# Kernel tuning notes

Hardware: AMD Instinct MI355X
Metric: run time of the kernel (lower is better)

Reference implementation:

```python
import jax, jax.numpy as jnp
import numpy as np

V, H, S, B, T = 32000, 1024, 512, 16, 128
SOS = 1  # config['special_tokens']['SOS'] assumed = 1


def setup_inputs() -> dict:
    key = jax.random.key(0)
    ks = jax.random.split(key, 16)
    s = 0.02
    return {
        "encoder_outputs": jax.random.normal(ks[0], (B, S, H), jnp.float32),
        "encoder_h": jax.random.normal(ks[1], (1, B, H), jnp.float32),
        "encoder_c": jax.random.normal(ks[2], (1, B, H), jnp.float32),
        "embedding": jax.random.normal(ks[3], (V, H), jnp.float32) * s,
        "Wq": jax.random.normal(ks[4], (H, H), jnp.float32) * s,
        "bq": jnp.zeros((H,), jnp.float32),
        "Wk": jax.random.normal(ks[5], (H, H), jnp.float32) * s,
        "bk": jnp.zeros((H,), jnp.float32),
        "Wv": jax.random.normal(ks[6], (H, H), jnp.float32) * s,
        "bv": jnp.zeros((H,), jnp.float32),
        "W_ih": jax.random.normal(ks[7], (4 * H, 2 * H), jnp.float32) * s,
        "b_ih": jnp.zeros((4 * H,), jnp.float32),
        "W_hh": jax.random.normal(ks[8], (4 * H, H), jnp.float32) * s,
        "b_hh": jnp.zeros((4 * H,), jnp.float32),
        "W_out": jax.random.normal(ks[9], (V, H), jnp.float32) * s,
        "b_out": jnp.zeros((V,), jnp.float32),
    }


def reference(encoder_outputs, encoder_h, encoder_c, embedding,
              Wq, bq, Wk, bk, Wv, bv,
              W_ih, b_ih, W_hh, b_hh, W_out, b_out):
    h0 = encoder_h[0]  # [B,H]
    c0 = encoder_c[0]
    # key/value projections of encoder outputs are constant across steps
    K = jnp.einsum('bsh,dh->bsd', encoder_outputs, Wk) + bk   # [B,S,H]
    Vl = jnp.einsum('bsh,dh->bsd', encoder_outputs, Wv) + bv  # [B,S,H]
    # decoder input is always SOS (source never updates it when target_tensor is None)
    emb = jnp.broadcast_to(embedding[SOS], (h0.shape[0], H))  # [B,H]
    scale = 1.0 / jnp.sqrt(jnp.float32(H))
    # 1x1 look-ahead mask (query seq_len == 1) is a no-op -> omitted

    def step(carry, _):
        h, c = carry
        q = h @ Wq.T + bq                                 # [B,H]
        scores = jnp.einsum('bh,bsh->bs', q, K) * scale   # [B,S]
        w = jax.nn.softmax(scores, axis=-1)
        ctx = jnp.einsum('bs,bsh->bh', w, Vl)             # [B,H]
        x = jnp.concatenate([emb, ctx], axis=-1)          # [B,2H] (embedded, attn)
        gates = x @ W_ih.T + b_ih + h @ W_hh.T + b_hh     # [B,4H]
        i, f, g, o = jnp.split(gates, 4, axis=-1)         # torch LSTM gate order i,f,g,o
        c2 = jax.nn.sigmoid(f) * c + jax.nn.sigmoid(i) * jnp.tanh(g)
        h2 = jax.nn.sigmoid(o) * jnp.tanh(c2)
        logits = h2 @ W_out.T + b_out                     # [B,V]
        return (h2, c2), logits

    (hT, cT), outs = jax.lax.scan(step, (h0, c0), None, length=T)  # outs [T,B,V]
    outs = jnp.transpose(outs, (1, 0, 2))                          # [B,T,V]
    log_probs = jax.nn.log_softmax(outs, axis=-1)
    return log_probs, (hT[None], cT[None])
```

## Files before the change

kernel.cpp:

```cpp
#include <hip/hip_runtime.h>
#include <hip/hip_bf16.h>
#include <math.h>

typedef short short8 __attribute__((ext_vector_type(8)));
typedef short short4v __attribute__((ext_vector_type(4)));
typedef float f32x4 __attribute__((ext_vector_type(4)));
typedef unsigned long long u64;

#define DEVI __device__ __forceinline__

DEVI float bf2f(short s){ union{unsigned u; float f;} x; x.u = ((unsigned)(unsigned short)s) << 16; return x.f; }

DEVI void st_u32v(unsigned* p, unsigned v){ __hip_atomic_store(p, v, __ATOMIC_RELAXED, __HIP_MEMORY_SCOPE_SYSTEM); }
DEVI u64  ld_u64v(const u64* p){ return __hip_atomic_load(p, __ATOMIC_RELAXED, __HIP_MEMORY_SCOPE_SYSTEM); }
DEVI unsigned bfbits(float f){ __hip_bfloat16 h = __float2bfloat16(f); unsigned short b; __builtin_memcpy(&b,&h,2); return (unsigned)b; }

constexpr size_t o_wout   = 0;
constexpr size_t o_encbf  = 0;
constexpr size_t o_kbf    = 16777216;
constexpr size_t o_wkbf   = 33554432;
constexpr size_t o_wvbf   = 35651584;
constexpr size_t o_wqtbf  = 37748736;
constexpr size_t o_vt     = 41943040;
constexpr size_t o_kq     = 65536000;
constexpr size_t o_vbf    = o_kq    + 16777216;
constexpr size_t o_wih2   = o_vbf   + 16777216;
constexpr size_t o_whh    = o_wih2  + 8388608;
constexpr size_t o_hall   = o_whh   + 8388608;
constexpr size_t o_gconst = o_hall  + 4194304;
constexpr size_t o_sb     = o_gconst+ 16384;
constexpr size_t o_hg     = o_sb    + 32768;
constexpr size_t o_ctxn   = o_hg    + 65536;
constexpr size_t o_eg     = o_ctxn  + 65536;

__global__ void k_convert(const float* __restrict__ src, __hip_bfloat16* __restrict__ dst, int n){
  int i = (blockIdx.x*blockDim.x + threadIdx.x)*4;
  int stride = gridDim.x*blockDim.x*4;
  for (; i < n; i += stride){
    float4 v = *(const float4*)(src+i);
    __hip_bfloat16 o[4] = {__float2bfloat16(v.x),__float2bfloat16(v.y),__float2bfloat16(v.z),__float2bfloat16(v.w)};
    *(short4v*)(dst+i) = *(const short4v*)o;
  }
}

__global__ void k_tcvt(const float* __restrict__ src, __hip_bfloat16* __restrict__ dst){
  __shared__ float tile[64][65];
  int i0 = blockIdx.y*64, j0 = blockIdx.x*64;
  int tr = threadIdx.x >> 6, tc = threadIdx.x & 63;
  for (int p=0;p<16;p++){ int r = p*4 + tr; tile[r][tc] = src[(size_t)(i0+r)*1024 + j0+tc]; }
  __syncthreads();
  for (int p=0;p<16;p++){ int r = p*4 + tr; dst[(size_t)(j0+r)*1024 + i0+tc] = __float2bfloat16(tile[tc][r]); }
}

__global__ void k_extract(const float* __restrict__ src, __hip_bfloat16* __restrict__ dst){
  int i = blockIdx.x*blockDim.x + threadIdx.x;
  int stride = gridDim.x*blockDim.x;
  for (; i < 4096*1024; i += stride){
    int r = i >> 10, c = i & 1023;
    dst[i] = __float2bfloat16(src[((size_t)r << 11) + 1024 + c]);
  }
}

__global__ void k_init(const float* __restrict__ eh, unsigned* __restrict__ h2,
                       unsigned* __restrict__ zbase){
  int i = blockIdx.x*blockDim.x + threadIdx.x;
  if (i < 16384) h2[i] = bfbits(eh[i]);
  if (i < 24576) zbase[i] = 0u;
}

__global__ void k_gconst(const float* __restrict__ emb, const float* __restrict__ Wih,
                         const float* __restrict__ bih, const float* __restrict__ bhh,
                         float* __restrict__ gc){
  int w = threadIdx.x >> 6, lane = threadIdx.x & 63;
  int n = blockIdx.x*4 + w;
  const float* er = emb + 1024;
  const float* wr = Wih + (size_t)n*2048;
  float acc = 0.f;
  for (int q=0;q<16;q++){ int k = lane*16+q; acc += er[k]*wr[k]; }
  for (int off=32; off; off>>=1) acc += __shfl_xor(acc, off);
  if (lane==0) gc[n] = acc + bih[n] + bhh[n];
}

__global__ void k_sb(const __hip_bfloat16* __restrict__ Kb, const float* __restrict__ bq,
                     float* __restrict__ sb){
  int w = threadIdx.x >> 6, lane = threadIdx.x & 63;
  int r = blockIdx.x*4 + w;
  const __hip_bfloat16* kr = Kb + (size_t)r*1024;
  float acc = 0.f;
  for (int q=0;q<16;q++){ int k = lane*16+q; acc += __bfloat162float(kr[k])*bq[k]; }
  for (int off=32; off; off>>=1) acc += __shfl_xor(acc, off);
  if (lane==0) sb[r] = acc * 0.03125f;
}

__global__ void k_vtrans(const __hip_bfloat16* __restrict__ V, __hip_bfloat16* __restrict__ VT){
  __shared__ short t[64][65];
  int b = blockIdx.z, s0 = blockIdx.y*64, h0 = blockIdx.x*64;
  int r = threadIdx.x >> 6, c = threadIdx.x & 63;
  const short* vp = (const short*)V + ((size_t)(b*512 + s0))*1024 + h0;
  #pragma unroll
  for (int p=0;p<16;p++) t[p*4+r][c] = vp[(size_t)(p*4+r)*1024 + c];
  __syncthreads();
  short* op = (short*)VT + ((size_t)(b*1024 + h0))*512 + s0;
  #pragma unroll
  for (int p=0;p<16;p++) op[(size_t)(p*4+r)*512 + c] = t[c][p*4+r];
}

template<int EPI>
__global__ __launch_bounds__(256) void k_gemm(const __hip_bfloat16* __restrict__ A,
    const __hip_bfloat16* __restrict__ Bm, const float* __restrict__ bias,
    void* __restrict__ Cp, int M, int N, int K, float scale){
  __shared__ __hip_bfloat16 sA[128*40];
  __shared__ __hip_bfloat16 sB[128*40];
  int tid = threadIdx.x;
  int lane = tid & 63, w = tid >> 6;
  int wr = w >> 1, wc = w & 1;
  int m0 = blockIdx.y*128, n0 = blockIdx.x*128;
  int lrow = lane & 15, lk = lane >> 4;
  f32x4 acc[4][4] = {};
  for (int k0 = 0; k0 < K; k0 += 32){
    __syncthreads();
    #pragma unroll
    for (int l0 = 0; l0 < 1024; l0 += 256){
      int l = l0 + tid;
      int half = l >> 9;
      int ch = l & 511;
      int row = ch >> 2, seg = ch & 3;
      const __hip_bfloat16* src = half ? (Bm + (size_t)(n0+row)*K + k0 + seg*8)
                                       : (A  + (size_t)(m0+row)*K + k0 + seg*8);
      __hip_bfloat16* dst = (half ? sB : sA) + row*40 + seg*8;
      *(short8*)dst = *(const short8*)src;
    }
    __syncthreads();
    short8 af[4], bfq[4];
    #pragma unroll
    for (int mi=0;mi<4;mi++) af[mi]  = *(short8*)(sA + (wr*64+mi*16+lrow)*40 + lk*8);
    #pragma unroll
    for (int ni=0;ni<4;ni++) bfq[ni] = *(short8*)(sB + (wc*64+ni*16+lrow)*40 + lk*8);
    #pragma unroll
    for (int mi=0;mi<4;mi++)
      #pragma unroll
      for (int ni=0;ni<4;ni++)
        acc[mi][ni] = __builtin_amdgcn_mfma_f32_16x16x32_bf16(af[mi], bfq[ni], acc[mi][ni], 0,0,0);
  }
  int crow0 = (lane>>4)*4;
  int ccol = lane & 15;
  #pragma unroll
  for (int mi=0;mi<4;mi++)
    #pragma unroll
    for (int ni=0;ni<4;ni++){
      int gn = n0 + wc*64 + ni*16 + ccol;
      float bv = bias ? bias[gn] : 0.0f;
      #pragma unroll
      for (int j=0;j<4;j++){
        int gm = m0 + wr*64 + mi*16 + crow0 + j;
        float v = acc[mi][ni][j]*scale + bv;
        if (EPI==0){
          ((__hip_bfloat16*)Cp)[(size_t)gm*N + gn] = __float2bfloat16(v);
        } else {
          int tt = gm >> 4, bb = gm & 15;
          ((float*)Cp)[(size_t)(bb*128+tt)*N + gn] = v;
        }
      }
    }
}

__global__ __launch_bounds__(256, 1) void k_decode(
    const __hip_bfloat16* __restrict__ KQ, const __hip_bfloat16* __restrict__ VT,
    const float* __restrict__ sb, const __hip_bfloat16* __restrict__ Whh,
    const __hip_bfloat16* __restrict__ Wih2, const float* __restrict__ gconst,
    const float* __restrict__ ec,
    unsigned* __restrict__ h2v, unsigned* __restrict__ egv,
    unsigned* __restrict__ ctx2v, __hip_bfloat16* __restrict__ hall,
    float* __restrict__ outH, float* __restrict__ outC)
{
  __shared__ __attribute__((aligned(16))) __hip_bfloat16 h4L[4][1032];
  __shared__ __attribute__((aligned(16))) float eL[528];
  __shared__ __attribute__((aligned(16))) float sPf[1024];
  __shared__ __attribute__((aligned(16))) __hip_bfloat16 sCtx[64];
  __shared__ float sSb[32];
  __shared__ float sGc[64];
  __shared__ float sRed[4];

  const int tid = threadIdx.x;
  const int lane = tid & 63, wv = tid >> 6;
  const int l16 = lane & 15, lhi = lane >> 4;
  const int blk = blockIdx.x;
  const int xcd = blk & 7, slot = blk >> 3;
  const int grp = xcd >> 1, half = xcd & 1;
  const int bloc = half*2 + (slot >> 4);
  const int chunk = slot & 15;
  const int g4 = grp*4;
  const int b = g4 + bloc;
  const int j0 = (half*32 + slot) * 16;

  short8 wfrag[64];
  {
    const __hip_bfloat16* wsrc = (wv < 2) ? Whh : Wih2;
    const int koff = (wv & 1) * 512;
    #pragma unroll
    for (int tt = 0; tt < 4; tt++)
      #pragma unroll
      for (int kt = 0; kt < 16; kt++)
        wfrag[tt*16+kt] = *(const short8*)(wsrc + (size_t)(tt*1024 + j0 + l16)*1024 + koff + kt*32 + lhi*8);
  }
  if (tid < 32) sSb[tid] = sb[b*512 + chunk*32 + tid];
  if (tid < 64) sGc[(tid>>4)*16 + (tid&15)] = gconst[(tid>>4)*1024 + j0 + (tid&15)];
  float creg = 0.f;
  if (tid < 64) creg = ec[(size_t)(g4 + (tid>>4))*1024 + j0 + (tid&15)];

  const __hip_bfloat16* kqBlk = KQ + ((size_t)(b*512 + chunk*32))*1024;
  const int ar = (l16 < 4) ? l16 : 3;
  const short8 zfrag = {};
  f32x4 gacc[4] = {};

  for (int st = 0; st < 128; ++st){
    const unsigned wantH = (unsigned)st;
    const unsigned wantE = (unsigned)(st+1);
    const unsigned wantC = (unsigned)(st+1);

    {
      const u64* s0 = (const u64*)(h2v + (size_t)b*1024) + tid*2;
      u64 a0, a1; bool ok;
      do {
        a0 = ld_u64v(s0); a1 = ld_u64v(s0+1);
        ok = (((unsigned)a0>>16)==wantH) && ((unsigned)(a0>>48)==wantH)
          && (((unsigned)a1>>16)==wantH) && ((unsigned)(a1>>48)==wantH);
      } while(!ok);
      short4v o = { (short)(unsigned)a0, (short)(a0>>32), (short)(unsigned)a1, (short)(a1>>32) };
      *(short4v*)&h4L[bloc][tid*4] = o;
    }
    __syncthreads();
    {
      int row = tid >> 3, kx = tid & 7;
      const __hip_bfloat16* kp = kqBlk + (size_t)row*1024 + kx*8;
      float acc = 0.f;
      #pragma unroll
      for (int q = 0; q < 16; q++){
        short8 kv = *(const short8*)(kp + q*64);
        short8 hv = *(const short8*)&h4L[bloc][kx*8 + q*64];
        #pragma unroll
        for (int e2 = 0; e2 < 8; e2++) acc += bf2f(hv[e2]) * bf2f(kv[e2]);
      }
      acc += __shfl_xor(acc, 1); acc += __shfl_xor(acc, 2); acc += __shfl_xor(acc, 4);
      if (kx == 0)
        st_u32v(&egv[b*512 + chunk*32 + row], bfbits(expf(acc + sSb[row])) | (wantE<<16));
    }
    {
      const u64* sp0 = (const u64*)(h2v + (size_t)(g4 + ((bloc+1)&3))*1024) + tid*2;
      const u64* sp1 = (const u64*)(h2v + (size_t)(g4 + ((bloc+2)&3))*1024) + tid*2;
      const u64* sp2 = (const u64*)(h2v + (size_t)(g4 + ((bloc+3)&3))*1024) + tid*2;
      u64 v[6]; bool ok;
      do {
        v[0]=ld_u64v(sp0); v[1]=ld_u64v(sp0+1);
        v[2]=ld_u64v(sp1); v[3]=ld_u64v(sp1+1);
        v[4]=ld_u64v(sp2); v[5]=ld_u64v(sp2+1);
        ok = true;
        #pragma unroll
        for (int i=0;i<6;i++) ok &= (((unsigned)v[i]>>16)==wantH) && ((unsigned)(v[i]>>48)==wantH);
      } while(!ok);
      #pragma unroll
      for (int rr=0;rr<3;rr++){
        int rl = (bloc+rr+1)&3;
        short4v o = { (short)(unsigned)v[rr*2], (short)(v[rr*2]>>32),
                      (short)(unsigned)v[rr*2+1], (short)(v[rr*2+1]>>32) };
        *(short4v*)&h4L[rl][tid*4] = o;
      }
    }
    __syncthreads();
    if (wv < 2){
      const int ko = (wv & 1) * 512;
      #pragma unroll
      for (int kt = 0; kt < 16; kt++){
        short8 a = *(const short8*)&h4L[ar][ko + kt*32 + lhi*8];
        a = (l16 < 4) ? a : zfrag;
        #pragma unroll
        for (int tt = 0; tt < 4; tt++)
          gacc[tt] = __builtin_amdgcn_mfma_f32_16x16x32_bf16(a, wfrag[tt*16+kt], gacc[tt], 0,0,0);
      }
    }

    {
      const u64* s = (const u64*)(egv + b*512) + tid;
      u64 v;
      do { v = ld_u64v(s); }
      while(!((((unsigned)v>>16)==wantE) && ((unsigned)(v>>48)==wantE)));
      float e0 = bf2f((short)(unsigned)v), e1 = bf2f((short)(v>>32));
      int i0 = tid*2;
      int pad = (i0>>7)<<2;
      eL[i0 + pad] = e0; eL[i0+1 + pad] = e1;
      float lp = e0 + e1;
      for (int off=32; off; off>>=1) lp += __shfl_xor(lp, off);
      if (lane == 0) sRed[wv] = lp;
    }
    __syncthreads();
    {
      float Linv = 1.0f/(sRed[0]+sRed[1]+sRed[2]+sRed[3]);
      int hloc = tid >> 2, sc = (tid & 3)*128;
      const __hip_bfloat16* vp = VT + ((size_t)(b*1024 + chunk*64 + hloc))*512 + sc;
      const float* ep = eL + sc + ((sc>>7)<<2);
      float a = 0.f;
      #pragma unroll
      for (int q = 0; q < 16; q++){
        short8 vv = *(const short8*)(vp + q*8);
        float4 e0 = *(const float4*)(ep + q*8);
        float4 e1 = *(const float4*)(ep + q*8 + 4);
        a += e0.x*bf2f(vv[0]) + e0.y*bf2f(vv[1]) + e0.z*bf2f(vv[2]) + e0.w*bf2f(vv[3]);
        a += e1.x*bf2f(vv[4]) + e1.y*bf2f(vv[5]) + e1.z*bf2f(vv[6]) + e1.w*bf2f(vv[7]);
      }
      a += __shfl_xor(a, 1); a += __shfl_xor(a, 2);
      if ((tid & 3) == 0) sCtx[hloc] = __float2bfloat16(a * Linv);
    }
    __syncthreads();
    if (tid < 64){
      unsigned short cbts; __builtin_memcpy(&cbts, &sCtx[tid], 2);
      st_u32v(&ctx2v[(size_t)b*1024 + chunk*64 + tid], (unsigned)cbts | (wantC<<16));
    }

    {
      int r = tid >> 6, c0 = (tid & 63)*16;
      const u64* s = (const u64*)(ctx2v + (size_t)(g4 + r)*1024 + c0);
      u64 v[8]; bool ok;
      do {
        ok = true;
        #pragma unroll
        for (int i=0;i<8;i++) v[i] = ld_u64v(s+i);
        #pragma unroll
        for (int i=0;i<8;i++) ok &= (((unsigned)v[i]>>16)==wantC) && ((unsigned)(v[i]>>48)==wantC);
      } while(!ok);
      short8 o0, o1;
      #pragma unroll
      for (int i=0;i<4;i++){ o0[2*i] = (short)(unsigned)v[i]; o0[2*i+1] = (short)(v[i]>>32); }
      #pragma unroll
      for (int i=0;i<4;i++){ o1[2*i] = (short)(unsigned)v[4+i]; o1[2*i+1] = (short)(v[4+i]>>32); }
      *(short8*)&h4L[r][c0] = o0;
      *(short8*)&h4L[r][c0+8] = o1;
    }
    __syncthreads();
    if (wv >= 2){
      const int ko = (wv & 1) * 512;
      #pragma unroll
      for (int kt = 0; kt < 16; kt++){
        short8 a = *(const short8*)&h4L[ar][ko + kt*32 + lhi*8];
        a = (l16 < 4) ? a : zfrag;
        #pragma unroll
        for (int tt = 0; tt < 4; tt++)
          gacc[tt] = __builtin_amdgcn_mfma_f32_16x16x32_bf16(a, wfrag[tt*16+kt], gacc[tt], 0,0,0);
      }
    }
    if (lhi == 0){
      #pragma unroll
      for (int tt = 0; tt < 4; tt++)
        *(f32x4*)&sPf[(wv*64 + tt*16 + l16)*4] = gacc[tt];
    }
    #pragma unroll
    for (int tt = 0; tt < 4; tt++) gacc[tt] = (f32x4){0.f,0.f,0.f,0.f};
    __syncthreads();
    if (tid < 64){
      int bb = tid >> 4, jj = tid & 15;
      float gv[4];
      #pragma unroll
      for (int tt = 0; tt < 4; tt++){
        float s = sGc[tt*16 + jj];
        #pragma unroll
        for (int w2 = 0; w2 < 4; w2++) s += sPf[(w2*64 + tt*16 + jj)*4 + bb];
        gv[tt] = s;
      }
      float si = 1.f/(1.f+expf(-gv[0]));
      float sf = 1.f/(1.f+expf(-gv[1]));
      float so = 1.f/(1.f+expf(-gv[3]));
      float c2 = sf*creg + si*tanhf(gv[2]);
      float h2 = so*tanhf(c2);
      creg = c2;
      int gb = g4 + bb;
      __hip_bfloat16 hbv = __float2bfloat16(h2);
      unsigned short hbits; __builtin_memcpy(&hbits, &hbv, 2);
      st_u32v(&h2v[(size_t)gb*1024 + j0 + jj], (unsigned)hbits | ((unsigned)(st+1)<<16));
      hall[((size_t)(st*16 + gb))*1024 + j0 + jj] = hbv;
      if (st == 127){ outH[gb*1024 + j0 + jj] = h2; outC[gb*1024 + j0 + jj] = c2; }
    }
  }
}

__global__ __launch_bounds__(256) void k_logsm(float* __restrict__ out){
  int row = blockIdx.x;
  float* p = out + (size_t)row*32000;
  int tid = threadIdx.x;
  __shared__ float red[4];
  float s = 0.f;
  for (int i = tid*4; i < 32000; i += 1024){
    float4 v = *(float4*)(p+i);
    s += __expf(v.x)+__expf(v.y)+__expf(v.z)+__expf(v.w);
  }
  for (int off=32; off; off>>=1) s += __shfl_xor(s, off);
  if ((tid&63)==0) red[tid>>6] = s;
  __syncthreads();
  float L = logf(red[0]+red[1]+red[2]+red[3]);
  for (int i = tid*4; i < 32000; i += 1024){
    float4 v = *(float4*)(p+i);
    v.x-=L; v.y-=L; v.z-=L; v.w-=L;
    *(float4*)(p+i) = v;
  }
}

extern "C" void kernel_launch(void* const* d_in, const int* in_sizes, int n_in,
                              void* d_out, int out_size, void* d_ws, size_t ws_size,
                              hipStream_t stream){
  const float* enc = (const float*)d_in[0];
  const float* eh  = (const float*)d_in[1];
  const float* ec  = (const float*)d_in[2];
  const float* emb = (const float*)d_in[3];
  const float* Wq  = (const float*)d_in[4];
  const float* bq  = (const float*)d_in[5];
  const float* Wk  = (const float*)d_in[6];
  const float* bk  = (const float*)d_in[7];
  const float* Wv  = (const float*)d_in[8];
  const float* bv  = (const float*)d_in[9];
  const float* Wih = (const float*)d_in[10];
  const float* bih = (const float*)d_in[11];
  const float* Whh = (const float*)d_in[12];
  const float* bhh = (const float*)d_in[13];
  const float* Wo  = (const float*)d_in[14];
  const float* bo  = (const float*)d_in[15];

  char* ws = (char*)d_ws;
  __hip_bfloat16* encbf = (__hip_bfloat16*)(ws + o_encbf);
  __hip_bfloat16* kbf   = (__hip_bfloat16*)(ws + o_kbf);
  __hip_bfloat16* wkbf  = (__hip_bfloat16*)(ws + o_wkbf);
  __hip_bfloat16* wvbf  = (__hip_bfloat16*)(ws + o_wvbf);
  __hip_bfloat16* wqtbf = (__hip_bfloat16*)(ws + o_wqtbf);
  __hip_bfloat16* vt    = (__hip_bfloat16*)(ws + o_vt);
  __hip_bfloat16* woutbf= (__hip_bfloat16*)(ws + o_wout);
  __hip_bfloat16* kq    = (__hip_bfloat16*)(ws + o_kq);
  __hip_bfloat16* vbf   = (__hip_bfloat16*)(ws + o_vbf);
  __hip_bfloat16* wih2  = (__hip_bfloat16*)(ws + o_wih2);
  __hip_bfloat16* whhbf = (__hip_bfloat16*)(ws + o_whh);
  __hip_bfloat16* hall  = (__hip_bfloat16*)(ws + o_hall);
  float* gconst = (float*)(ws + o_gconst);
  float* sbp    = (float*)(ws + o_sb);
  unsigned* h2v   = (unsigned*)(ws + o_hg);
  unsigned* ctx2v = (unsigned*)(ws + o_ctxn);
  unsigned* egv   = (unsigned*)(ws + o_eg);
  float* outP   = (float*)d_out;
  float* outH   = outP + 65536000;
  float* outC   = outH + 16384;

  k_convert<<<1024,256,0,stream>>>(enc, encbf, 8388608);
  k_convert<<<256,256,0,stream>>>(Wk, wkbf, 1048576);
  k_convert<<<256,256,0,stream>>>(Wv, wvbf, 1048576);
  k_tcvt<<<dim3(16,16),256,0,stream>>>(Wq, wqtbf);
  k_gemm<0><<<dim3(8,64),256,0,stream>>>(encbf, wkbf, bk, kbf, 8192,1024,1024, 1.f);
  k_gemm<0><<<dim3(8,64),256,0,stream>>>(encbf, wvbf, bv, vbf, 8192,1024,1024, 1.f);
  k_gemm<0><<<dim3(8,64),256,0,stream>>>(kbf, wqtbf, (const float*)nullptr, kq, 8192,1024,1024, 0.03125f);
  k_vtrans<<<dim3(16,8,16),256,0,stream>>>(vbf, vt);
  k_sb<<<2048,256,0,stream>>>(kbf, bq, sbp);
  k_extract<<<1024,256,0,stream>>>(Wih, wih2);
  k_convert<<<1024,256,0,stream>>>(Whh, whhbf, 4194304);
  k_gconst<<<1024,256,0,stream>>>(emb, Wih, bih, bhh, gconst);
  k_init<<<96,256,0,stream>>>(eh, h2v, ctx2v);

  {
    const __hip_bfloat16* a_kq = kq; const __hip_bfloat16* a_vt = vt;
    const float* a_sb = sbp; const __hip_bfloat16* a_whh = whhbf;
    const __hip_bfloat16* a_wih = wih2; const float* a_gc = gconst;
    const float* a_ec = ec;
    unsigned* a_h = h2v; unsigned* a_e = egv; unsigned* a_c = ctx2v;
    __hip_bfloat16* a_ha = hall;
    float* a_oh = outH; float* a_oc = outC;
    void* args[] = { &a_kq, &a_vt, &a_sb, &a_whh, &a_wih, &a_gc, &a_ec,
                     &a_h, &a_e, &a_c, &a_ha, &a_oh, &a_oc };
    hipError_t err = hipLaunchCooperativeKernel((void*)k_decode, dim3(256), dim3(256),
                                                args, 0u, stream);
    if (err != hipSuccess){
      k_decode<<<256,256,0,stream>>>(kq, vt, sbp, whhbf, wih2, gconst, ec,
                                     h2v, egv, ctx2v, hall, outH, outC);
    }
  }

  k_convert<<<2048,256,0,stream>>>(Wo, woutbf, 32768000);
  k_gemm<1><<<dim3(250,16),256,0,stream>>>(hall, woutbf, bo, d_out, 2048,32000,1024, 1.f);
  k_logsm<<<2048,256,0,stream>>>(outP);
}
```

Before: 2.733 ms.

## Decouple attention batch ownership from gate group and overlap W_hh gates with next step

Each block now runs attention for its own batch row (bown) but computes LSTM gates for a different group of four rows (gg = ga+2). This lets the recurrent W_hh·h contribution for the next step be computed right after h is published, instead of waiting on the critical path next to the context. The h/e/ctx exchange buffers are double-buffered by step parity, and the W_hh vs W_ih wave roles are swapped. It adds an extra grid-wide h wait and synchronisation per step, plus more flag traffic across XCDs.

```diff
diff --git a/kernel.cpp b/kernel.cpp
--- a/kernel.cpp
+++ b/kernel.cpp
@@ -29,9 +29,9 @@
 constexpr size_t o_hall   = o_whh   + 8388608;
 constexpr size_t o_gconst = o_hall  + 4194304;
 constexpr size_t o_sb     = o_gconst+ 16384;
-constexpr size_t o_hg     = o_sb    + 32768;
-constexpr size_t o_ctxn   = o_hg    + 65536;
-constexpr size_t o_eg     = o_ctxn  + 65536;
+constexpr size_t o_hv     = o_sb    + 32768;
+constexpr size_t o_ev     = o_hv    + 131072;
+constexpr size_t o_cv     = o_ev    + 65536;
 
 __global__ void k_convert(const float* __restrict__ src, __hip_bfloat16* __restrict__ dst, int n){
   int i = (blockIdx.x*blockDim.x + threadIdx.x)*4;
@@ -61,11 +61,10 @@
   }
 }
 
-__global__ void k_init(const float* __restrict__ eh, unsigned* __restrict__ h2,
-                       unsigned* __restrict__ zbase){
+__global__ void k_init(const float* __restrict__ eh, unsigned* __restrict__ base){
   int i = blockIdx.x*blockDim.x + threadIdx.x;
-  if (i < 16384) h2[i] = bfbits(eh[i]);
-  if (i < 24576) zbase[i] = 0u;
+  if (i < 16384) base[i] = bfbits(eh[i]);
+  else if (i < 81920) base[i] = 0u;
 }
 
 __global__ void k_gconst(const float* __restrict__ emb, const float* __restrict__ Wih,
@@ -169,8 +168,8 @@
     const float* __restrict__ sb, const __hip_bfloat16* __restrict__ Whh,
     const __hip_bfloat16* __restrict__ Wih2, const float* __restrict__ gconst,
     const float* __restrict__ ec,
-    unsigned* __restrict__ h2v, unsigned* __restrict__ egv,
-    unsigned* __restrict__ ctx2v, __hip_bfloat16* __restrict__ hall,
+    unsigned* __restrict__ hv, unsigned* __restrict__ ev,
+    unsigned* __restrict__ cv, __hip_bfloat16* __restrict__ hall,
     float* __restrict__ outH, float* __restrict__ outC)
 {
   __shared__ __attribute__((aligned(16))) __hip_bfloat16 h4L[4][1032];
@@ -186,16 +185,16 @@
   const int l16 = lane & 15, lhi = lane >> 4;
   const int blk = blockIdx.x;
   const int xcd = blk & 7, slot = blk >> 3;
-  const int grp = xcd >> 1, half = xcd & 1;
-  const int bloc = half*2 + (slot >> 4);
+  const int ga = xcd >> 1, half = xcd & 1;
+  const int bown = ga*4 + half*2 + (slot >> 4);
   const int chunk = slot & 15;
-  const int g4 = grp*4;
-  const int b = g4 + bloc;
+  const int gg = (ga + 2) & 3;
+  const int g4 = gg*4;
   const int j0 = (half*32 + slot) * 16;
 
   short8 wfrag[64];
   {
-    const __hip_bfloat16* wsrc = (wv < 2) ? Whh : Wih2;
+    const __hip_bfloat16* wsrc = (wv >= 2) ? Whh : Wih2;
     const int koff = (wv & 1) * 512;
     #pragma unroll
     for (int tt = 0; tt < 4; tt++)
@@ -203,23 +202,61 @@
       for (int kt = 0; kt < 16; kt++)
         wfrag[tt*16+kt] = *(const short8*)(wsrc + (size_t)(tt*1024 + j0 + l16)*1024 + koff + kt*32 + lhi*8);
   }
-  if (tid < 32) sSb[tid] = sb[b*512 + chunk*32 + tid];
+  if (tid < 32) sSb[tid] = sb[bown*512 + chunk*32 + tid];
   if (tid < 64) sGc[(tid>>4)*16 + (tid&15)] = gconst[(tid>>4)*1024 + j0 + (tid&15)];
   float creg = 0.f;
   if (tid < 64) creg = ec[(size_t)(g4 + (tid>>4))*1024 + j0 + (tid&15)];
 
-  const __hip_bfloat16* kqBlk = KQ + ((size_t)(b*512 + chunk*32))*1024;
+  const __hip_bfloat16* kqBlk = KQ + ((size_t)(bown*512 + chunk*32))*1024;
   const int ar = (l16 < 4) ? l16 : 3;
   const short8 zfrag = {};
   f32x4 gacc[4] = {};
 
+  {
+    int r = tid >> 6, c0 = (tid & 63)*16;
+    const u64* s = (const u64*)(hv + (size_t)(g4 + r)*1024 + c0);
+    u64 v[8]; bool ok;
+    do {
+      ok = true;
+      #pragma unroll
+      for (int i=0;i<8;i++) v[i] = ld_u64v(s+i);
+      #pragma unroll
+      for (int i=0;i<8;i++) ok &= (((unsigned)v[i]>>16)==0u) && ((unsigned)(v[i]>>48)==0u);
+    } while(!ok);
+    #pragma unroll
+    for (int i=0;i<8;i++){
+      short2 o = { (short)(unsigned)v[i], (short)(v[i]>>32) };
+      *(short2*)&h4L[r][c0 + 2*i] = *(short2*)&o;
+    }
+  }
+  __syncthreads();
+  if (wv >= 2){
+    const int ko = (wv & 1) * 512;
+    #pragma unroll
+    for (int kt = 0; kt < 16; kt++){
+      short8 a = *(const short8*)&h4L[ar][ko + kt*32 + lhi*8];
+      a = (l16 < 4) ? a : zfrag;
+      #pragma unroll
+      for (int tt = 0; tt < 4; tt++)
+        gacc[tt] = __builtin_amdgcn_mfma_f32_16x16x32_bf16(a, wfrag[tt*16+kt], gacc[tt], 0,0,0);
+    }
+    if (lhi == 0){
+      #pragma unroll
+      for (int tt = 0; tt < 4; tt++)
+        *(f32x4*)&sPf[(wv*64 + tt*16 + l16)*4] = gacc[tt];
+    }
+    #pragma unroll
+    for (int tt = 0; tt < 4; tt++) gacc[tt] = (f32x4){0.f,0.f,0.f,0.f};
+  }
+  __syncthreads();
+
   for (int st = 0; st < 128; ++st){
+    const int p0 = st & 1, p1 = (st+1) & 1;
     const unsigned wantH = (unsigned)st;
-    const unsigned wantE = (unsigned)(st+1);
-    const unsigned wantC = (unsigned)(st+1);
+    const unsigned wantN = (unsigned)(st+1);
 
     {
-      const u64* s0 = (const u64*)(h2v + (size_t)b*1024) + tid*2;
+      const u64* s0 = (const u64*)(hv + (size_t)p0*16384 + (size_t)bown*1024) + tid*2;
       u64 a0, a1; bool ok;
       do {
         a0 = ld_u64v(s0); a1 = ld_u64v(s0+1);
@@ -227,7 +264,7 @@
           && (((unsigned)a1>>16)==wantH) && ((unsigned)(a1>>48)==wantH);
       } while(!ok);
       short4v o = { (short)(unsigned)a0, (short)(a0>>32), (short)(unsigned)a1, (short)(a1>>32) };
-      *(short4v*)&h4L[bloc][tid*4] = o;
+      *(short4v*)&h4L[0][tid*4] = o;
     }
     __syncthreads();
     {
@@ -237,56 +274,22 @@
       #pragma unroll
       for (int q = 0; q < 16; q++){
         short8 kv = *(const short8*)(kp + q*64);
-        short8 hv = *(const short8*)&h4L[bloc][kx*8 + q*64];
-        #pragma unroll
-        for (int e2 = 0; e2 < 8; e2++) acc += bf2f(hv[e2]) * bf2f(kv[e2]);
+        short8 hv8 = *(const short8*)&h4L[0][kx*8 + q*64];
+        #pragma unroll
+        for (int e2 = 0; e2 < 8; e2++) acc += bf2f(hv8[e2]) * bf2f(kv[e2]);
       }
       acc += __shfl_xor(acc, 1); acc += __shfl_xor(acc, 2); acc += __shfl_xor(acc, 4);
       if (kx == 0)
-        st_u32v(&egv[b*512 + chunk*32 + row], bfbits(expf(acc + sSb[row])) | (wantE<<16));
-    }
+        st_u32v(&ev[(size_t)p1*8192 + bown*512 + chunk*32 + row], bfbits(expf(acc + sSb[row])) | (wantN<<16));
+    }
+
     {
-      const u64* sp0 = (const u64*)(h2v + (size_t)(g4 + ((bloc+1)&3))*1024) + tid*2;
-      const u64* sp1 = (const u64*)(h2v + (size_t)(g4 + ((bloc+2)&3))*1024) + tid*2;
-      const u64* sp2 = (const u64*)(h2v + (size_t)(g4 + ((bloc+3)&3))*1024) + tid*2;
-      u64 v[6]; bool ok;
-      do {
-        v[0]=ld_u64v(sp0); v[1]=ld_u64v(sp0+1);
-        v[2]=ld_u64v(sp1); v[3]=ld_u64v(sp1+1);
-        v[4]=ld_u64v(sp2); v[5]=ld_u64v(sp2+1);
-        ok = true;
-        #pragma unroll
-        for (int i=0;i<6;i++) ok &= (((unsigned)v[i]>>16)==wantH) && ((unsigned)(v[i]>>48)==wantH);
-      } while(!ok);
-      #pragma unroll
-      for (int rr=0;rr<3;rr++){
-        int rl = (bloc+rr+1)&3;
-        short4v o = { (short)(unsigned)v[rr*2], (short)(v[rr*2]>>32),
-                      (short)(unsigned)v[rr*2+1], (short)(v[rr*2+1]>>32) };
-        *(short4v*)&h4L[rl][tid*4] = o;
-      }
-    }
-    __syncthreads();
-    if (wv < 2){
-      const int ko = (wv & 1) * 512;
-      #pragma unroll
-      for (int kt = 0; kt < 16; kt++){
-        short8 a = *(const short8*)&h4L[ar][ko + kt*32 + lhi*8];
-        a = (l16 < 4) ? a : zfrag;
-        #pragma unroll
-        for (int tt = 0; tt < 4; tt++)
-          gacc[tt] = __builtin_amdgcn_mfma_f32_16x16x32_bf16(a, wfrag[tt*16+kt], gacc[tt], 0,0,0);
-      }
-    }
-
-    {
-      const u64* s = (const u64*)(egv + b*512) + tid;
+      const u64* s = (const u64*)(ev + (size_t)p1*8192 + bown*512) + tid;
       u64 v;
       do { v = ld_u64v(s); }
-      while(!((((unsigned)v>>16)==wantE) && ((unsigned)(v>>48)==wantE)));
+      while(!((((unsigned)v>>16)==wantN) && ((unsigned)(v>>48)==wantN)));
       float e0 = bf2f((short)(unsigned)v), e1 = bf2f((short)(v>>32));
-      int i0 = tid*2;
-      int pad = (i0>>7)<<2;
+      int i0 = tid*2, pad = (tid>>6)<<2;
       eL[i0 + pad] = e0; eL[i0+1 + pad] = e1;
       float lp = e0 + e1;
       for (int off=32; off; off>>=1) lp += __shfl_xor(lp, off);
@@ -296,14 +299,14 @@
     {
       float Linv = 1.0f/(sRed[0]+sRed[1]+sRed[2]+sRed[3]);
       int hloc = tid >> 2, sc = (tid & 3)*128;
-      const __hip_bfloat16* vp = VT + ((size_t)(b*1024 + chunk*64 + hloc))*512 + sc;
-      const float* ep = eL + sc + ((sc>>7)<<2);
+      const __hip_bfloat16* vp = VT + ((size_t)(bown*1024 + chunk*64 + hloc))*512 + sc;
+      const float* epp = eL + sc + ((sc>>7)<<2);
       float a = 0.f;
       #pragma unroll
       for (int q = 0; q < 16; q++){
         short8 vv = *(const short8*)(vp + q*8);
-        float4 e0 = *(const float4*)(ep + q*8);
-        float4 e1 = *(const float4*)(ep + q*8 + 4);
+        float4 e0 = *(const float4*)(epp + q*8);
+        float4 e1 = *(const float4*)(epp + q*8 + 4);
         a += e0.x*bf2f(vv[0]) + e0.y*bf2f(vv[1]) + e0.z*bf2f(vv[2]) + e0.w*bf2f(vv[3]);
         a += e1.x*bf2f(vv[4]) + e1.y*bf2f(vv[5]) + e1.z*bf2f(vv[6]) + e1.w*bf2f(vv[7]);
       }
@@ -313,30 +316,28 @@
     __syncthreads();
     if (tid < 64){
       unsigned short cbts; __builtin_memcpy(&cbts, &sCtx[tid], 2);
-      st_u32v(&ctx2v[(size_t)b*1024 + chunk*64 + tid], (unsigned)cbts | (wantC<<16));
+      st_u32v(&cv[(size_t)p1*16384 + (size_t)bown*1024 + chunk*64 + tid], (unsigned)cbts | (wantN<<16));
     }
 
     {
       int r = tid >> 6, c0 = (tid & 63)*16;
-      const u64* s = (const u64*)(ctx2v + (size_t)(g4 + r)*1024 + c0);
+      const u64* s = (const u64*)(cv + (size_t)p1*16384 + (size_t)(g4 + r)*1024 + c0);
       u64 v[8]; bool ok;
       do {
         ok = true;
         #pragma unroll
         for (int i=0;i<8;i++) v[i] = ld_u64v(s+i);
         #pragma unroll
-        for (int i=0;i<8;i++) ok &= (((unsigned)v[i]>>16)==wantC) && ((unsigned)(v[i]>>48)==wantC);
+        for (int i=0;i<8;i++) ok &= (((unsigned)v[i]>>16)==wantN) && ((unsigned)(v[i]>>48)==wantN);
       } while(!ok);
-      short8 o0, o1;
-      #pragma unroll
-      for (int i=0;i<4;i++){ o0[2*i] = (short)(unsigned)v[i]; o0[2*i+1] = (short)(v[i]>>32); }
-      #pragma unroll
-      for (int i=0;i<4;i++){ o1[2*i] = (short)(unsigned)v[4+i]; o1[2*i+1] = (short)(v[4+i]>>32); }
-      *(short8*)&h4L[r][c0] = o0;
-      *(short8*)&h4L[r][c0+8] = o1;
-    }
-    __syncthreads();
-    if (wv >= 2){
+      #pragma unroll
+      for (int i=0;i<8;i++){
+        short2 o = { (short)(unsigned)v[i], (short)(v[i]>>32) };
+        *(short2*)&h4L[r][c0 + 2*i] = *(short2*)&o;
+      }
+    }
+    __syncthreads();
+    if (wv < 2){
       const int ko = (wv & 1) * 512;
       #pragma unroll
       for (int kt = 0; kt < 16; kt++){
@@ -346,14 +347,14 @@
         for (int tt = 0; tt < 4; tt++)
           gacc[tt] = __builtin_amdgcn_mfma_f32_16x16x32_bf16(a, wfrag[tt*16+kt], gacc[tt], 0,0,0);
       }
-    }
-    if (lhi == 0){
-      #pragma unroll
-      for (int tt = 0; tt < 4; tt++)
-        *(f32x4*)&sPf[(wv*64 + tt*16 + l16)*4] = gacc[tt];
-    }
-    #pragma unroll
-    for (int tt = 0; tt < 4; tt++) gacc[tt] = (f32x4){0.f,0.f,0.f,0.f};
+      if (lhi == 0){
+        #pragma unroll
+        for (int tt = 0; tt < 4; tt++)
+          *(f32x4*)&sPf[(wv*64 + tt*16 + l16)*4] = gacc[tt];
+      }
+      #pragma unroll
+      for (int tt = 0; tt < 4; tt++) gacc[tt] = (f32x4){0.f,0.f,0.f,0.f};
+    }
     __syncthreads();
     if (tid < 64){
       int bb = tid >> 4, jj = tid & 15;
@@ -372,11 +373,51 @@
       float h2 = so*tanhf(c2);
       creg = c2;
       int gb = g4 + bb;
-      __hip_bfloat16 hbv = __float2bfloat16(h2);
-      unsigned short hbits; __builtin_memcpy(&hbits, &hbv, 2);
-      st_u32v(&h2v[(size_t)gb*1024 + j0 + jj], (unsigned)hbits | ((unsigned)(st+1)<<16));
+      unsigned hb = bfbits(h2);
+      st_u32v(&hv[(size_t)p1*16384 + (size_t)gb*1024 + j0 + jj], hb | (wantN<<16));
+      __hip_bfloat16 hbv; unsigned short hu = (unsigned short)hb; __builtin_memcpy(&hbv, &hu, 2);
       hall[((size_t)(st*16 + gb))*1024 + j0 + jj] = hbv;
       if (st == 127){ outH[gb*1024 + j0 + jj] = h2; outC[gb*1024 + j0 + jj] = c2; }
+    }
+
+    if (st < 127){
+      {
+        int r = tid >> 6, c0 = (tid & 63)*16;
+        const u64* s = (const u64*)(hv + (size_t)p1*16384 + (size_t)(g4 + r)*1024 + c0);
+        u64 v[8]; bool ok;
+        do {
+          ok = true;
+          #pragma unroll
+          for (int i=0;i<8;i++) v[i] = ld_u64v(s+i);
+          #pragma unroll
+          for (int i=0;i<8;i++) ok &= (((unsigned)v[i]>>16)==wantN) && ((unsigned)(v[i]>>48)==wantN);
+        } while(!ok);
+        #pragma unroll
+        for (int i=0;i<8;i++){
+          short2 o = { (short)(unsigned)v[i], (short)(v[i]>>32) };
+          *(short2*)&h4L[r][c0 + 2*i] = *(short2*)&o;
+        }
+      }
+      __syncthreads();
+      if (wv >= 2){
+        const int ko = (wv & 1) * 512;
+        #pragma unroll
+        for (int kt = 0; kt < 16; kt++){
+          short8 a = *(const short8*)&h4L[ar][ko + kt*32 + lhi*8];
+          a = (l16 < 4) ? a : zfrag;
+          #pragma unroll
+          for (int tt = 0; tt < 4; tt++)
+            gacc[tt] = __builtin_amdgcn_mfma_f32_16x16x32_bf16(a, wfrag[tt*16+kt], gacc[tt], 0,0,0);
+        }
+        if (lhi == 0){
+          #pragma unroll
+          for (int tt = 0; tt < 4; tt++)
+            *(f32x4*)&sPf[(wv*64 + tt*16 + l16)*4] = gacc[tt];
+        }
+        #pragma unroll
+        for (int tt = 0; tt < 4; tt++) gacc[tt] = (f32x4){0.f,0.f,0.f,0.f};
+      }
+      __syncthreads();
     }
   }
 }
@@ -437,9 +478,9 @@
   __hip_bfloat16* hall  = (__hip_bfloat16*)(ws + o_hall);
   float* gconst = (float*)(ws + o_gconst);
   float* sbp    = (float*)(ws + o_sb);
-  unsigned* h2v   = (unsigned*)(ws + o_hg);
-  unsigned* ctx2v = (unsigned*)(ws + o_ctxn);
-  unsigned* egv   = (unsigned*)(ws + o_eg);
+  unsigned* hvp = (unsigned*)(ws + o_hv);
+  unsigned* evp = (unsigned*)(ws + o_ev);
+  unsigned* cvp = (unsigned*)(ws + o_cv);
   float* outP   = (float*)d_out;
   float* outH   = outP + 65536000;
   float* outC   = outH + 16384;
@@ -456,14 +497,14 @@
   k_extract<<<1024,256,0,stream>>>(Wih, wih2);
   k_convert<<<1024,256,0,stream>>>(Whh, whhbf, 4194304);
   k_gconst<<<1024,256,0,stream>>>(emb, Wih, bih, bhh, gconst);
-  k_init<<<96,256,0,stream>>>(eh, h2v, ctx2v);
+  k_init<<<320,256,0,stream>>>(eh, hvp);
 
   {
     const __hip_bfloat16* a_kq = kq; const __hip_bfloat16* a_vt = vt;
     const float* a_sb = sbp; const __hip_bfloat16* a_whh = whhbf;
     const __hip_bfloat16* a_wih = wih2; const float* a_gc = gconst;
     const float* a_ec = ec;
-    unsigned* a_h = h2v; unsigned* a_e = egv; unsigned* a_c = ctx2v;
+    unsigned* a_h = hvp; unsigned* a_e = evp; unsigned* a_c = cvp;
     __hip_bfloat16* a_ha = hall;
     float* a_oh = outH; float* a_oc = outC;
     void* args[] = { &a_kq, &a_vt, &a_sb, &a_whh, &a_wih, &a_gc, &a_ec,
@@ -472,7 +513,7 @@
                                                 args, 0u, stream);
     if (err != hipSuccess){
       k_decode<<<256,256,0,stream>>>(kq, vt, sbp, whhbf, wih2, gconst, ec,
-                                     h2v, egv, ctx2v, hall, outH, outC);
+                                     hvp, evp, cvp, hall, outH, outC);
     }
   }
 
```

Result: slower. 2.795 ms (+2.3%).
